# Performance work log

Measured on AMD Instinct MI355X. Metric: run time of the kernel, lower is better.

Reference implementation:

```python
import jax, jax.numpy as jnp
import numpy as np

B, N, P_FEATS = 8, 4096, 3
WIDTH, HEADS, LAYERS, N_LAT = 768, 12, 8, 256
NUM_FREQS = 8
D_HEAD = WIDTH // HEADS
SCALE = 1.0 / np.sqrt(np.sqrt(D_HEAD))  # applied to q and k separately
IN_DIM = 3 * (1 + 2 * NUM_FREQS) + P_FEATS  # 54
EPS = 1e-5


def fourier_embed(pc):
    # pc: [B,N,3] -> [B,N,51] (include_input + sin/cos at freqs 2^0..2^7)
    freqs = (2.0 ** jnp.arange(NUM_FREQS)).astype(pc.dtype)
    ang = pc[..., None] * freqs  # [B,N,3,F]
    ang = ang.reshape(*pc.shape[:-1], 3 * NUM_FREQS)
    return jnp.concatenate([pc, jnp.sin(ang), jnp.cos(ang)], axis=-1)


def layernorm(x, s, b):
    mu = jnp.mean(x, axis=-1, keepdims=True)
    var = jnp.mean(jnp.square(x - mu), axis=-1, keepdims=True)
    return (x - mu) * jax.lax.rsqrt(var + EPS) * s + b


def mh_attn(q, k, v):
    # q: [B,T,H,C], k/v: [B,S,H,C]
    w = jnp.einsum('bthc,bshc->bhts', q * SCALE, k * SCALE)
    w = jax.nn.softmax(w.astype(jnp.float32), axis=-1).astype(q.dtype)
    out = jnp.einsum('bhts,bshc->bthc', w, v)
    return out.reshape(*q.shape[:2], -1)


def setup_inputs() -> dict:
    key = jax.random.key(0)
    ks = iter(jax.random.split(key, 64))
    rn = lambda shape, std=0.02: jax.random.normal(next(ks), shape, jnp.float32) * std
    inp = {
        'pc': jax.random.normal(next(ks), (B, N, 3), jnp.float32),
        'feats': jax.random.uniform(next(ks), (B, N, P_FEATS), jnp.float32),
        'query': rn((N_LAT, WIDTH)),
        'in_W': rn((WIDTH, IN_DIM)), 'in_b': jnp.zeros((WIDTH,)),
        'ca_qkv_W': rn((3 * WIDTH, WIDTH)), 'ca_qkv_b': jnp.zeros((3 * WIDTH,)),
        'ca_proj_W': rn((WIDTH, WIDTH)), 'ca_proj_b': jnp.zeros((WIDTH,)),
        'ln1_s': jnp.ones((LAYERS, WIDTH)), 'ln1_b': jnp.zeros((LAYERS, WIDTH)),
        'qkv_W': rn((LAYERS, 3 * WIDTH, WIDTH)), 'qkv_b': jnp.zeros((LAYERS, 3 * WIDTH)),
        'proj_W': rn((LAYERS, WIDTH, WIDTH)), 'proj_b': jnp.zeros((LAYERS, WIDTH)),
        'ln2_s': jnp.ones((LAYERS, WIDTH)), 'ln2_b': jnp.zeros((LAYERS, WIDTH)),
        'fc_W': rn((LAYERS, 4 * WIDTH, WIDTH)), 'fc_b': jnp.zeros((LAYERS, 4 * WIDTH)),
        'fc2_W': rn((LAYERS, WIDTH, 4 * WIDTH)), 'fc2_b': jnp.zeros((LAYERS, WIDTH)),
    }
    return inp


def _forward(pc, feats, query, in_W, in_b, ca_qkv_W, ca_qkv_b, ca_proj_W, ca_proj_b,
             ln1_s, ln1_b, qkv_W, qkv_b, proj_W, proj_b, ln2_s, ln2_b,
             fc_W, fc_b, fc2_W, fc2_b):
    bs = pc.shape[0]
    data = jnp.concatenate([fourier_embed(pc), feats], axis=-1)  # [B,N,54]
    data = data @ in_W.T + in_b  # [B,N,W]
    q_lat = jnp.broadcast_to(query[None], (bs, N_LAT, WIDTH))

    # --- cross attention (no residual, matching source) ---
    q = (q_lat @ ca_qkv_W.T + ca_qkv_b)[..., :WIDTH]
    kv = data @ ca_qkv_W.T + ca_qkv_b
    k, v = kv[..., WIDTH:2 * WIDTH], kv[..., 2 * WIDTH:]
    q = q.reshape(bs, N_LAT, HEADS, D_HEAD)
    k = k.reshape(bs, N, HEADS, D_HEAD)
    v = v.reshape(bs, N, HEADS, D_HEAD)
    latents = mh_attn(q, k, v) @ ca_proj_W.T + ca_proj_b  # [B,L,W]

    # --- self-attention transformer stack via scan ---
    def block(x, p):
        (l1s, l1b, qW, qb, pW, pb, l2s, l2b, fW, fb, f2W, f2b) = p
        h = layernorm(x, l1s, l1b)
        qkv = (h @ qW.T + qb).reshape(bs, N_LAT, HEADS, 3 * D_HEAD)
        qh, kh, vh = jnp.split(qkv, 3, axis=-1)
        x = x + mh_attn(qh, kh, vh) @ pW.T + pb
        h = layernorm(x, l2s, l2b)
        h = jax.nn.gelu(h @ fW.T + fb, approximate=False) @ f2W.T + f2b
        return x + h, None

    params = (ln1_s, ln1_b, qkv_W, qkv_b, proj_W, proj_b, ln2_s, ln2_b, fc_W, fc_b, fc2_W, fc2_b)
    latents, _ = jax.lax.scan(block, latents, params)
    return latents, pc


def reference(pc, feats, query, in_W, in_b, ca_qkv_W, ca_qkv_b, ca_proj_W, ca_proj_b,
              ln1_s, ln1_b, qkv_W, qkv_b, proj_W, proj_b, ln2_s, ln2_b,
              fc_W, fc_b, fc2_W, fc2_b):
    return _forward(pc, feats, query, in_W, in_b, ca_qkv_W, ca_qkv_b, ca_proj_W, ca_proj_b,
                    ln1_s, ln1_b, qkv_W, qkv_b, proj_W, proj_b, ln2_s, ln2_b,
                    fc_W, fc_b, fc2_W, fc2_b)
```

## Files before the change

kernel.cpp:

```cpp
#include <hip/hip_runtime.h>
#include <stdint.h>

typedef unsigned short u16;
typedef __bf16 bf16x8 __attribute__((ext_vector_type(8)));
typedef float f32x4 __attribute__((ext_vector_type(4)));

#define DEVINL __device__ __forceinline__

DEVINL u16 f2bf(float f) {
  union { float f; unsigned u; } c; c.f = f;
  unsigned u = c.u + 0x7FFFu + ((c.u >> 16) & 1u);
  return (u16)(u >> 16);
}

DEVINL float bf2f(u16 v) {
  union { unsigned u; float f; } c; c.u = (unsigned)v << 16;
  return c.f;
}

DEVINL unsigned pk2bf(float a, float b) {
#if __has_builtin(__builtin_amdgcn_cvt_pk_bf16_f32)
  auto r = __builtin_amdgcn_cvt_pk_bf16_f32(a, b);
  unsigned u;
  __builtin_memcpy(&u, &r, 4);
  return u;
#else
  return (unsigned)f2bf(a) | ((unsigned)f2bf(b) << 16);
#endif
}

DEVINL void gl2lds16(const void* g, void* l) {
  __builtin_amdgcn_global_load_lds(
      (const __attribute__((address_space(1))) unsigned int*)g,
      (__attribute__((address_space(3))) unsigned int*)l, 16, 0, 0);
}

__global__ __launch_bounds__(256) void cvt4_kernel(
    const float* __restrict__ s0, u16* __restrict__ d0, int n0,
    const float* __restrict__ s1, u16* __restrict__ d1, int n1,
    const float* __restrict__ s2, u16* __restrict__ d2, int n2,
    const float* __restrict__ s3, u16* __restrict__ d3, int n3) {
  int i = blockIdx.x * 256 + threadIdx.x;
  const float* s; u16* d;
  if (i < n0) { s = s0; d = d0; }
  else {
    i -= n0;
    if (i < n1) { s = s1; d = d1; }
    else {
      i -= n1;
      if (i < n2) { s = s2; d = d2; }
      else {
        i -= n2;
        if (i >= n3) return;
        s = s3; d = d3;
      }
    }
  }
  float4 v = ((const float4*)s)[i];
  ((uint2*)d)[i] = make_uint2(pk2bf(v.x, v.y), pk2bf(v.z, v.w));
}

__global__ __launch_bounds__(256) void pad_inwT_kernel(const float* __restrict__ src,
                                                       u16* __restrict__ dst) {
  int t = blockIdx.x * 256 + threadIdx.x;
  if (t >= 64 * 768) return;
  int j = t / 768, o = t - j * 768;
  dst[t] = (j < 54) ? f2bf(src[o * 54 + j]) : (u16)0;
}

__global__ __launch_bounds__(256) void bprime_kernel(const float* __restrict__ caW,
                                                     const float* __restrict__ caB,
                                                     const float* __restrict__ inb,
                                                     float* __restrict__ bp) {
  int w = threadIdx.x >> 6, lane = threadIdx.x & 63;
  int m = blockIdx.x * 4 + w;
  const float* row = caW + (size_t)(768 + m) * 768;
  float s = 0.f;
#pragma unroll
  for (int k = 0; k < 12; k++) s += row[lane + k * 64] * inb[lane + k * 64];
#pragma unroll
  for (int msk = 32; msk >= 1; msk >>= 1) s += __shfl_xor(s, msk, 64);
  if (lane == 0) bp[m] = s + caB[768 + m];
}

__global__ __launch_bounds__(256) void embed_kernel(const float* __restrict__ pc,
                                                    const float* __restrict__ feats,
                                                    u16* __restrict__ emb) {
  int t = blockIdx.x * 256 + threadIdx.x;
  int p = t >> 6, c = t & 63;
  float v = 0.f;
  if (c < 3) {
    v = pc[p * 3 + c];
  } else if (c < 27) {
    int i = c - 3;
    float f = (float)(1 << (i & 7));
    v = sinf(pc[p * 3 + (i >> 3)] * f);
  } else if (c < 51) {
    int i = c - 27;
    float f = (float)(1 << (i & 7));
    v = cosf(pc[p * 3 + (i >> 3)] * f);
  } else if (c < 54) {
    v = feats[p * 3 + (c - 51)];
  }
  emb[t] = f2bf(v);
}

template <int TM, int TN, int WR, int WC, int MODE>
__global__ __launch_bounds__(256) void gemm_t(
    const u16* __restrict__ A, const u16* __restrict__ Bw,
    const float* __restrict__ bias, const float* __restrict__ resid,
    float* __restrict__ outF, u16* __restrict__ outB,
    int M, int N, int Nout, int K, int gelu,
    u16* __restrict__ vt, int vy, int skvt, int bsh) {
  constexpr int IM = TM / WR / 16;
  constexpr int IN = TN / WC / 16;
  __shared__ u16 As[TM * 32];
  __shared__ u16 Bs[TN * 32];
  const int tid = threadIdx.x;
  const int lane = tid & 63, w = tid >> 6;
  const int l15 = lane & 15, quad = lane >> 4;
  const int mblk = blockIdx.x * TM, nblk = blockIdx.y * TN;
  const int wm = (w % WR) * (TM / WR);
  const int wn = (w / WR) * (TN / WC);

  f32x4 acc[IM][IN];
#pragma unroll
  for (int i = 0; i < IM; i++)
#pragma unroll
    for (int j = 0; j < IN; j++) acc[i][j] = f32x4{0.f, 0.f, 0.f, 0.f};

  bool tv = false;
  if (MODE == 1) tv = ((int)blockIdx.y >= vy);
  if (MODE == 2) tv = ((int)(blockIdx.y % 3) == 2);

  if (!tv) {
    for (int k0 = 0; k0 < K; k0 += 32) {
#pragma unroll
      for (int s = tid; s < TM * 4; s += 256) {
        int row = s >> 2, c8 = (s & 3) << 3;
        gl2lds16(A + (size_t)(mblk + row) * K + (k0 + c8), &As[s * 8]);
      }
#pragma unroll
      for (int s = tid; s < TN * 4; s += 256) {
        int row = s >> 2, c8 = (s & 3) << 3;
        gl2lds16(Bw + (size_t)(nblk + row) * K + (k0 + c8), &Bs[s * 8]);
      }
      __syncthreads();
      bf16x8 af[IM], bfr[IN];
#pragma unroll
      for (int i = 0; i < IM; i++)
        af[i] = *(const bf16x8*)&As[(wm + i * 16 + l15) * 32 + quad * 8];
#pragma unroll
      for (int j = 0; j < IN; j++)
        bfr[j] = *(const bf16x8*)&Bs[(wn + j * 16 + l15) * 32 + quad * 8];
#pragma unroll
      for (int i = 0; i < IM; i++)
#pragma unroll
        for (int j = 0; j < IN; j++)
          acc[i][j] = __builtin_amdgcn_mfma_f32_16x16x32_bf16(bfr[j], af[i], acc[i][j], 0, 0, 0);
      __syncthreads();
    }
#pragma unroll
    for (int i = 0; i < IM; i++) {
      int m = mblk + wm + i * 16 + l15;
#pragma unroll
      for (int j = 0; j < IN; j++) {
        int n0 = nblk + wn + j * 16 + quad * 4;
        float4 bv = bias ? *(const float4*)&bias[n0] : make_float4(0.f, 0.f, 0.f, 0.f);
        float v0 = acc[i][j][0] + bv.x;
        float v1 = acc[i][j][1] + bv.y;
        float v2 = acc[i][j][2] + bv.z;
        float v3 = acc[i][j][3] + bv.w;
        if (gelu) {
          v0 = 0.5f * v0 * (1.0f + erff(v0 * 0.70710678118f));
          v1 = 0.5f * v1 * (1.0f + erff(v1 * 0.70710678118f));
          v2 = 0.5f * v2 * (1.0f + erff(v2 * 0.70710678118f));
          v3 = 0.5f * v3 * (1.0f + erff(v3 * 0.70710678118f));
        }
        size_t idx = (size_t)m * Nout + n0;
        if (resid) {
          float4 rv = *(const float4*)&resid[idx];
          v0 += rv.x; v1 += rv.y; v2 += rv.z; v3 += rv.w;
        }
        if (outF) {
          float4 ov = {v0, v1, v2, v3};
          *(float4*)&outF[idx] = ov;
        }
        if (outB) {
          *(uint2*)&outB[idx] = make_uint2(pk2bf(v0, v1), pk2bf(v2, v3));
        }
      }
    }
  } else {
    for (int k0 = 0; k0 < K; k0 += 32) {
#pragma unroll
      for (int s = tid; s < TM * 4; s += 256) {
        int row = s >> 2, c8 = (s & 3) << 3;
        gl2lds16(A + (size_t)(mblk + row) * K + (k0 + c8), &As[s * 8]);
      }
#pragma unroll
      for (int s = tid; s < TN * 4; s += 256) {
        int row = s >> 2, c8 = (s & 3) << 3;
        gl2lds16(Bw + (size_t)(nblk + row) * K + (k0 + c8), &Bs[s * 8]);
      }
      __syncthreads();
      bf16x8 af[IM], bfr[IN];
#pragma unroll
      for (int i = 0; i < IM; i++)
        af[i] = *(const bf16x8*)&As[(wm + i * 16 + l15) * 32 + quad * 8];
#pragma unroll
      for (int j = 0; j < IN; j++)
        bfr[j] = *(const bf16x8*)&Bs[(wn + j * 16 + l15) * 32 + quad * 8];
#pragma unroll
      for (int i = 0; i < IM; i++)
#pragma unroll
        for (int j = 0; j < IN; j++)
          acc[i][j] = __builtin_amdgcn_mfma_f32_16x16x32_bf16(af[i], bfr[j], acc[i][j], 0, 0, 0);
      __syncthreads();
    }
    int msk = (1 << bsh) - 1;
#pragma unroll
    for (int j = 0; j < IN; j++) {
      int n = nblk + wn + j * 16 + l15;
      float bv = bias ? bias[n] : 0.f;
#pragma unroll
      for (int i = 0; i < IM; i++) {
        int m0 = mblk + wm + i * 16 + quad * 4;
        int b = m0 >> bsh;
        int s0 = m0 & msk;
        float v0 = acc[i][j][0] + bv;
        float v1 = acc[i][j][1] + bv;
        float v2 = acc[i][j][2] + bv;
        float v3 = acc[i][j][3] + bv;
        size_t vrow;
        if (MODE == 2) {
          int h = blockIdx.y / 3;
          vrow = (size_t)(b * 12 + h) * 64 + (wn + j * 16 + l15);
        } else {
          vrow = (size_t)b * 768 + (n - vy * TN);
        }
        size_t addr = vrow * skvt + s0;
        *(uint2*)&vt[addr] = make_uint2(pk2bf(v0, v1), pk2bf(v2, v3));
      }
    }
  }
}

__global__ __launch_bounds__(256) void flash_kernel(
    const u16* __restrict__ Q, long qb, int qrs, int qhs,
    const u16* __restrict__ Kp, long kb, int krs, int khs,
    const u16* __restrict__ Vt, u16* __restrict__ Out,
    u16* __restrict__ Part, float* __restrict__ Ml,
    int Skv, int nsplit, int kvlen, int nbh, float scale2) {
  __shared__ u16 Qs[64 * 64];
  __shared__ u16 Ks[64 * 64];
  __shared__ u16 Vs[64 * 64];
  __shared__ u16 Ps[64 * 72];

  const int tid = threadIdx.x;
  const int lane = tid & 63, w = tid >> 6;
  const int l15 = lane & 15, quad = lane >> 4;

  int bid = blockIdx.x;
  int grp = nbh * nsplit;
  int qt = bid / grp;
  int rem = bid - qt * grp;
  int bh = rem / nsplit;
  int split = rem - bh * nsplit;
  int h = bh % 12, b = bh / 12;

  const u16* Qbase = Q + (size_t)b * qb + (size_t)(qt * 64) * qrs + h * qhs;
  const u16* Kbase = Kp + (size_t)b * kb + (size_t)h * khs;
  const u16* Vbase = Vt + ((size_t)(b * 12 + h) * 64) * Skv;

#pragma unroll
  for (int p = 0; p < 2; ++p) {
    int slot = tid + p * 256;
    int row = slot >> 3, c = slot & 7;
    int cg = (c - row) & 7;
    gl2lds16(Qbase + (size_t)row * qrs + cg * 8, &Qs[slot * 8]);
  }
  __syncthreads();

  bf16x8 qa[2];
#pragma unroll
  for (int kk = 0; kk < 2; kk++)
    qa[kk] = *(const bf16x8*)&Qs[(w * 16 + l15) * 64 + ((kk * 4 + quad + l15) & 7) * 8];

  f32x4 zero = {0.f, 0.f, 0.f, 0.f};
  f32x4 O[4];
#pragma unroll
  for (int d = 0; d < 4; d++) O[d] = zero;
  float m_i = -1e30f, l_i = 0.f;

  int kt0 = split * kvlen;
  for (int kt = kt0; kt < kt0 + kvlen; kt += 64) {
#pragma unroll
    for (int p = 0; p < 2; ++p) {
      int slot = tid + p * 256;
      int row = slot >> 3, c = slot & 7;
      int cg = (c - row) & 7;
      gl2lds16(Kbase + (size_t)(kt + row) * krs + cg * 8, &Ks[slot * 8]);
      gl2lds16(Vbase + (size_t)row * Skv + kt + cg * 8, &Vs[slot * 8]);
    }
    __syncthreads();

    f32x4 St[4];
#pragma unroll
    for (int j = 0; j < 4; j++) St[j] = zero;
#pragma unroll
    for (int kk = 0; kk < 2; kk++) {
#pragma unroll
      for (int j = 0; j < 4; j++) {
        bf16x8 kf = *(const bf16x8*)&Ks[(j * 16 + l15) * 64 + ((kk * 4 + quad + l15) & 7) * 8];
        St[j] = __builtin_amdgcn_mfma_f32_16x16x32_bf16(kf, qa[kk], St[j], 0, 0, 0);
      }
    }

    float mx = St[0][0];
#pragma unroll
    for (int j = 0; j < 4; j++)
#pragma unroll
      for (int r = 0; r < 4; r++) mx = fmaxf(mx, St[j][r]);
    mx = fmaxf(mx, __shfl_xor(mx, 16, 64));
    mx = fmaxf(mx, __shfl_xor(mx, 32, 64));
    mx *= scale2;
    float mnew = fmaxf(m_i, mx);
    float al = __expf(m_i - mnew);
    m_i = mnew;
    float sum = 0.f;
#pragma unroll
    for (int j = 0; j < 4; j++) {
      float p0 = __expf(fmaf(St[j][0], scale2, -mnew));
      float p1 = __expf(fmaf(St[j][1], scale2, -mnew));
      float p2 = __expf(fmaf(St[j][2], scale2, -mnew));
      float p3 = __expf(fmaf(St[j][3], scale2, -mnew));
      sum += (p0 + p1) + (p2 + p3);
      *(uint2*)&Ps[(w * 16 + l15) * 72 + j * 16 + quad * 4] =
          make_uint2(pk2bf(p0, p1), pk2bf(p2, p3));
    }
    sum += __shfl_xor(sum, 16, 64);
    sum += __shfl_xor(sum, 32, 64);
    l_i = l_i * al + sum;

    float a0 = __shfl(al, quad * 20 + 0, 64);
    float a1 = __shfl(al, quad * 20 + 1, 64);
    float a2 = __shfl(al, quad * 20 + 2, 64);
    float a3 = __shfl(al, quad * 20 + 3, 64);
#pragma unroll
    for (int d = 0; d < 4; d++) {
      O[d][0] *= a0; O[d][1] *= a1; O[d][2] *= a2; O[d][3] *= a3;
    }
    __asm__ __volatile__("s_waitcnt lgkmcnt(0)" ::: "memory");
#pragma unroll
    for (int kk = 0; kk < 2; kk++) {
      bf16x8 pa = *(const bf16x8*)&Ps[(w * 16 + l15) * 72 + kk * 32 + quad * 8];
#pragma unroll
      for (int d = 0; d < 4; d++) {
        bf16x8 vf = *(const bf16x8*)&Vs[(d * 16 + l15) * 64 + ((kk * 4 + quad + l15) & 7) * 8];
        O[d] = __builtin_amdgcn_mfma_f32_16x16x32_bf16(pa, vf, O[d], 0, 0, 0);
      }
    }
    __syncthreads();
  }

  float l0 = __shfl(l_i, quad * 20 + 0, 64);
  float l1 = __shfl(l_i, quad * 20 + 1, 64);
  float l2 = __shfl(l_i, quad * 20 + 2, 64);
  float l3 = __shfl(l_i, quad * 20 + 3, 64);

  if (nsplit == 1) {
    float inv0 = 1.f / l0, inv1 = 1.f / l1, inv2 = 1.f / l2, inv3 = 1.f / l3;
    u16* Ob = Out + ((size_t)(b * 256 + qt * 64 + w * 16 + quad * 4)) * 768 + h * 64 + l15;
#pragma unroll
    for (int d = 0; d < 4; d++) {
      Ob[(size_t)0 * 768 + d * 16] = f2bf(O[d][0] * inv0);
      Ob[(size_t)1 * 768 + d * 16] = f2bf(O[d][1] * inv1);
      Ob[(size_t)2 * 768 + d * 16] = f2bf(O[d][2] * inv2);
      Ob[(size_t)3 * 768 + d * 16] = f2bf(O[d][3] * inv3);
    }
  } else {
    float m0 = __shfl(m_i, quad * 20 + 0, 64);
    float m1 = __shfl(m_i, quad * 20 + 1, 64);
    float m2 = __shfl(m_i, quad * 20 + 2, 64);
    float m3 = __shfl(m_i, quad * 20 + 3, 64);
    u16* Pb = Part + ((size_t)(bh * 4 + qt) * nsplit + split) * 4096;
    int rowb = w * 16 + quad * 4;
#pragma unroll
    for (int d = 0; d < 4; d++) {
      Pb[(rowb + 0) * 64 + d * 16 + l15] = f2bf(O[d][0]);
      Pb[(rowb + 1) * 64 + d * 16 + l15] = f2bf(O[d][1]);
      Pb[(rowb + 2) * 64 + d * 16 + l15] = f2bf(O[d][2]);
      Pb[(rowb + 3) * 64 + d * 16 + l15] = f2bf(O[d][3]);
    }
    if (l15 == 0) {
      float* MlB = Ml + ((size_t)(bh * 4 + qt) * nsplit + split) * 128;
      MlB[rowb + 0] = m0; MlB[rowb + 1] = m1; MlB[rowb + 2] = m2; MlB[rowb + 3] = m3;
      MlB[64 + rowb + 0] = l0; MlB[64 + rowb + 1] = l1;
      MlB[64 + rowb + 2] = l2; MlB[64 + rowb + 3] = l3;
    }
  }
}

__global__ __launch_bounds__(256) void freduce_kernel(
    const u16* __restrict__ Part, const float* __restrict__ Ml,
    u16* __restrict__ Out, int nsplit) {
  int bid = blockIdx.x;
  int qt = bid & 3, bh = bid >> 2;
  int h = bh % 12, b = bh / 12;
  int tid = threadIdx.x;
  int r = tid >> 2, dc = tid & 3;
  const float* mlb = Ml + (size_t)(bh * 4 + qt) * nsplit * 128;
  float M = -1e30f;
  for (int s = 0; s < nsplit; s++) M = fmaxf(M, mlb[s * 128 + r]);
  float L = 0.f;
  float accv[16];
#pragma unroll
  for (int i = 0; i < 16; i++) accv[i] = 0.f;
  const u16* pb = Part + (size_t)(bh * 4 + qt) * nsplit * 4096 + r * 64 + dc * 16;
  for (int s = 0; s < nsplit; s++) {
    float wgt = __expf(mlb[s * 128 + r] - M);
    L += wgt * mlb[s * 128 + 64 + r];
    u16 tmp[16];
    *(uint4*)tmp = *(const uint4*)(pb + s * 4096);
    *(uint4*)(tmp + 8) = *(const uint4*)(pb + s * 4096 + 8);
#pragma unroll
    for (int i = 0; i < 16; i++) accv[i] += wgt * bf2f(tmp[i]);
  }
  float inv = 1.f / L;
  unsigned ot[8];
#pragma unroll
  for (int i = 0; i < 8; i++)
    ot[i] = pk2bf(accv[2 * i] * inv, accv[2 * i + 1] * inv);
  u16* ob = Out + ((size_t)(b * 256 + qt * 64 + r)) * 768 + h * 64 + dc * 16;
  *(uint4*)ob = *(uint4*)ot;
  *(uint4*)(ob + 8) = *(uint4*)(ot + 4);
}

__global__ __launch_bounds__(256) void ln_kernel(const float* __restrict__ X,
                                                 const float* __restrict__ sc,
                                                 const float* __restrict__ bi,
                                                 u16* __restrict__ Hout) {
  int row = blockIdx.x;
  int tid = threadIdx.x;
  const float* x = X + (size_t)row * 768;
  float v0 = x[tid], v1 = x[tid + 256], v2 = x[tid + 512];
  float s = v0 + v1 + v2;
  float q = v0 * v0 + v1 * v1 + v2 * v2;
#pragma unroll
  for (int m = 1; m < 64; m <<= 1) {
    s += __shfl_xor(s, m, 64);
    q += __shfl_xor(q, m, 64);
  }
  __shared__ float rs[4], rq[4];
  if ((tid & 63) == 0) { rs[tid >> 6] = s; rq[tid >> 6] = q; }
  __syncthreads();
  s = rs[0] + rs[1] + rs[2] + rs[3];
  q = rq[0] + rq[1] + rq[2] + rq[3];
  float mu = s * (1.f / 768.f);
  float var = q * (1.f / 768.f) - mu * mu;
  float rstd = rsqrtf(var + 1e-5f);
  u16* ho = Hout + (size_t)row * 768;
  ho[tid]       = f2bf((v0 - mu) * rstd * sc[tid]       + bi[tid]);
  ho[tid + 256] = f2bf((v1 - mu) * rstd * sc[tid + 256] + bi[tid + 256]);
  ho[tid + 512] = f2bf((v2 - mu) * rstd * sc[tid + 512] + bi[tid + 512]);
}

__global__ __launch_bounds__(256) void copy4_kernel(const float* __restrict__ src,
                                                    float* __restrict__ dst, int n4) {
  int i = blockIdx.x * 256 + threadIdx.x;
  if (i < n4) ((float4*)dst)[i] = ((const float4*)src)[i];
}

extern "C" void kernel_launch(void* const* d_in, const int* in_sizes, int n_in,
                              void* d_out, int out_size, void* d_ws, size_t ws_size,
                              hipStream_t stream) {
  const float* pc        = (const float*)d_in[0];
  const float* feats     = (const float*)d_in[1];
  const float* query     = (const float*)d_in[2];
  const float* in_W      = (const float*)d_in[3];
  const float* in_b      = (const float*)d_in[4];
  const float* ca_qkv_W  = (const float*)d_in[5];
  const float* ca_qkv_b  = (const float*)d_in[6];
  const float* ca_proj_W = (const float*)d_in[7];
  const float* ca_proj_b = (const float*)d_in[8];
  const float* ln1_s     = (const float*)d_in[9];
  const float* ln1_b     = (const float*)d_in[10];
  const float* qkv_W     = (const float*)d_in[11];
  const float* qkv_b     = (const float*)d_in[12];
  const float* proj_W    = (const float*)d_in[13];
  const float* proj_b    = (const float*)d_in[14];
  const float* ln2_s     = (const float*)d_in[15];
  const float* ln2_b     = (const float*)d_in[16];
  const float* fc_W      = (const float*)d_in[17];
  const float* fc_b      = (const float*)d_in[18];
  const float* fc2_W     = (const float*)d_in[19];
  const float* fc2_b     = (const float*)d_in[20];

  char* base = (char*)d_ws;
  size_t off = 0;
  auto alloc = [&](size_t bytes) -> char* {
    char* p = base + off;
    off += (bytes + 255) & ~(size_t)255;
    return p;
  };

  u16* WqT     = (u16*)alloc(64 * 768 * 2);
  u16* Wquery  = (u16*)alloc(256 * 768 * 2);
  u16* Wcaqkv  = (u16*)alloc(2304 * 768 * 2);
  u16* Wcaproj = (u16*)alloc(768 * 768 * 2);
  u16* Wkp     = (u16*)alloc(1536 * 64 * 2);
  float* bprime = (float*)alloc(1536 * 4);
  u16* qc      = (u16*)alloc(256 * 768 * 2);
  u16* attn    = (u16*)alloc((size_t)2048 * 768 * 2);
  u16* hbuf    = (u16*)alloc((size_t)2048 * 768 * 2);
  char* uni    = alloc(13369344);
  u16* qkvb    = (u16*)uni;
  u16* VtS     = (u16*)(uni + 9437184);
  u16* fc1     = (u16*)uni;
  u16* Part    = (u16*)uni;
  float* Ml    = (float*)(uni + 12582912);

  size_t fixed_end = off;
  const size_t wAllSz = (size_t)8 * (2304 * 768 + 768 * 768 + 2 * 3072 * 768) * 2;
  auto crossSz = [](int cb) {
    return (size_t)cb * 4096 * 64 * 2 + 2 * ((size_t)cb * 4096 * 768 * 2);
  };

  bool allw; int CB;
  if (fixed_end + (wAllSz > crossSz(8) ? wAllSz : crossSz(8)) + 65536 <= ws_size) {
    allw = true;  CB = 8;
  } else if (fixed_end + 14155776 + crossSz(2) + 65536 <= ws_size) {
    allw = false; CB = 2;
  } else {
    allw = false; CB = 1;
  }

  u16 *WqkvB, *WprojB, *WfcB, *Wfc2B, *emb, *kvbK, *VtC;
  if (allw) {
    char* X = base + off;
    WqkvB  = (u16*)X;
    WprojB = WqkvB + (size_t)8 * 2304 * 768;
    WfcB   = WprojB + (size_t)8 * 768 * 768;
    Wfc2B  = WfcB + (size_t)8 * 3072 * 768;
    emb  = (u16*)X;
    kvbK = (u16*)(X + (size_t)CB * 4096 * 64 * 2);
    VtC  = (u16*)(X + (size_t)CB * 4096 * 64 * 2 + (size_t)CB * 4096 * 768 * 2);
  } else {
    WqkvB  = (u16*)alloc(2304 * 768 * 2);
    WprojB = (u16*)alloc(768 * 768 * 2);
    WfcB   = (u16*)alloc(3072 * 768 * 2);
    Wfc2B  = (u16*)alloc((size_t)768 * 3072 * 2);
    emb  = (u16*)alloc((size_t)CB * 4096 * 64 * 2);
    kvbK = (u16*)alloc((size_t)CB * 4096 * 768 * 2);
    VtC  = (u16*)alloc((size_t)CB * 4096 * 768 * 2);
  }

  float* latents = (float*)d_out;
  const float scale2 = 0.125f;

  {
    int n0 = 256 * 768 / 4, n1 = 2304 * 768 / 4, n2 = 768 * 768 / 4;
    cvt4_kernel<<<(n0 + n1 + n2 + 255) / 256, 256, 0, stream>>>(
        query, Wquery, n0, ca_qkv_W, Wcaqkv, n1, ca_proj_W, Wcaproj, n2,
        nullptr, nullptr, 0);
  }
  pad_inwT_kernel<<<192, 256, 0, stream>>>(in_W, WqT);
  gemm_t<64, 64, 2, 2, 0><<<dim3(24, 1), 256, 0, stream>>>(
      Wcaqkv + (size_t)768 * 768, WqT, nullptr, nullptr, nullptr, Wkp,
      1536, 64, 64, 768, 0, nullptr, 0, 0, 0);
  bprime_kernel<<<384, 256, 0, stream>>>(ca_qkv_W, ca_qkv_b, in_b, bprime);

  gemm_t<64, 64, 2, 2, 0><<<dim3(4, 12), 256, 0, stream>>>(
      Wquery, Wcaqkv, ca_qkv_b, nullptr, nullptr, qc,
      256, 768, 768, 768, 0, nullptr, 0, 0, 0);

  int nchunk = 8 / CB;
  for (int c = 0; c < nchunk; ++c) {
    int Mc = CB * 4096;
    const float* pc_c = pc + (size_t)c * Mc * 3;
    const float* ft_c = feats + (size_t)c * Mc * 3;
    embed_kernel<<<Mc / 4, 256, 0, stream>>>(pc_c, ft_c, emb);
    gemm_t<128, 128, 2, 2, 1><<<dim3(Mc / 128, 12), 256, 0, stream>>>(
        emb, Wkp, bprime, nullptr, nullptr, kvbK,
        Mc, 1536, 768, 64, 0, VtC, 6, 4096, 12);
    flash_kernel<<<CB * 12 * 16, 256, 0, stream>>>(
        qc, 0L, 768, 64, kvbK, (long)4096 * 768, 768, 64, VtC,
        nullptr, Part, Ml, 4096, 4, 1024, CB * 12, scale2);
    freduce_kernel<<<CB * 48, 256, 0, stream>>>(
        Part, Ml, attn + (size_t)c * CB * 256 * 768, 4);
  }
  gemm_t<64, 64, 2, 2, 0><<<dim3(32, 12), 256, 0, stream>>>(
      attn, Wcaproj, ca_proj_b, nullptr, latents, nullptr,
      2048, 768, 768, 768, 0, nullptr, 0, 0, 0);

  if (allw) {
    int n0 = 8 * 2304 * 768 / 4, n1 = 8 * 768 * 768 / 4, n2 = 8 * 3072 * 768 / 4;
    cvt4_kernel<<<(n0 + n1 + 2 * n2 + 255) / 256, 256, 0, stream>>>(
        qkv_W, WqkvB, n0, proj_W, WprojB, n1, fc_W, WfcB, n2, fc2_W, Wfc2B, n2);
  }

  for (int l = 0; l < 8; ++l) {
    u16* Wlq  = allw ? WqkvB  + (size_t)l * 2304 * 768 : WqkvB;
    u16* Wlp  = allw ? WprojB + (size_t)l * 768 * 768  : WprojB;
    u16* Wlf  = allw ? WfcB   + (size_t)l * 3072 * 768 : WfcB;
    u16* Wlf2 = allw ? Wfc2B  + (size_t)l * 3072 * 768 : Wfc2B;
    if (!allw) {
      int n0 = 2304 * 768 / 4, n1 = 768 * 768 / 4, n2 = 3072 * 768 / 4;
      cvt4_kernel<<<(n0 + n1 + 2 * n2 + 255) / 256, 256, 0, stream>>>(
          qkv_W + (size_t)l * 2304 * 768, Wlq, n0,
          proj_W + (size_t)l * 768 * 768, Wlp, n1,
          fc_W + (size_t)l * 3072 * 768, Wlf, n2,
          fc2_W + (size_t)l * 768 * 3072, Wlf2, n2);
    }
    ln_kernel<<<2048, 256, 0, stream>>>(latents, ln1_s + l * 768, ln1_b + l * 768, hbuf);
    gemm_t<64, 64, 2, 2, 2><<<dim3(32, 36), 256, 0, stream>>>(
        hbuf, Wlq, qkv_b + l * 2304, nullptr, nullptr, qkvb,
        2048, 2304, 2304, 768, 0, VtS, 0, 256, 8);
    flash_kernel<<<384, 256, 0, stream>>>(
        qkvb, (long)256 * 2304, 2304, 192, qkvb + 64, (long)256 * 2304, 2304, 192,
        VtS, attn, nullptr, nullptr, 256, 1, 256, 96, scale2);
    gemm_t<64, 64, 2, 2, 0><<<dim3(32, 12), 256, 0, stream>>>(
        attn, Wlp, proj_b + l * 768, latents, latents, nullptr,
        2048, 768, 768, 768, 0, nullptr, 0, 0, 0);
    ln_kernel<<<2048, 256, 0, stream>>>(latents, ln2_s + l * 768, ln2_b + l * 768, hbuf);
    gemm_t<64, 128, 1, 4, 0><<<dim3(32, 24), 256, 0, stream>>>(
        hbuf, Wlf, fc_b + l * 3072, nullptr, nullptr, fc1,
        2048, 3072, 3072, 768, 1, nullptr, 0, 0, 0);
    gemm_t<64, 64, 2, 2, 0><<<dim3(32, 12), 256, 0, stream>>>(
        fc1, Wlf2, fc2_b + l * 768, latents, latents, nullptr,
        2048, 768, 768, 3072, 0, nullptr, 0, 0, 0);
  }

  copy4_kernel<<<96, 256, 0, stream>>>(pc, (float*)d_out + (size_t)2048 * 768, 98304 / 4);
}
```

Before: 1.333 ms.

## Add split-K GEMMs for narrow projections and double-buffer flash attention K/V

```diff
diff --git a/kernel.cpp b/kernel.cpp
--- a/kernel.cpp
+++ b/kernel.cpp
@@ -33,6 +33,15 @@
   __builtin_amdgcn_global_load_lds(
       (const __attribute__((address_space(1))) unsigned int*)g,
       (__attribute__((address_space(3))) unsigned int*)l, 16, 0, 0);
+}
+
+template <int N> DEVINL void waitvm() {
+  asm volatile("s_waitcnt vmcnt(%0)" ::"n"(N) : "memory");
+}
+DEVINL void bar() {
+  asm volatile("" ::: "memory");
+  __builtin_amdgcn_s_barrier();
+  asm volatile("" ::: "memory");
 }
 
 __global__ __launch_bounds__(256) void cvt4_kernel(
@@ -246,6 +255,93 @@
   }
 }
 
+template <int TM, int TN, int WR, int WC>
+__global__ __launch_bounds__(256) void gemmsk_t(
+    const u16* __restrict__ A, const u16* __restrict__ Bw,
+    float* __restrict__ P, int M, int N, int K, int kchunk) {
+  constexpr int IM = TM / WR / 16;
+  constexpr int IN = TN / WC / 16;
+  __shared__ u16 As[TM * 32];
+  __shared__ u16 Bs[TN * 32];
+  const int tid = threadIdx.x;
+  const int lane = tid & 63, w = tid >> 6;
+  const int l15 = lane & 15, quad = lane >> 4;
+  const int mblk = blockIdx.x * TM, nblk = blockIdx.y * TN;
+  const int wm = (w % WR) * (TM / WR);
+  const int wn = (w / WR) * (TN / WC);
+  const int kbeg = blockIdx.z * kchunk;
+  const int kend = kbeg + kchunk;
+
+  f32x4 acc[IM][IN];
+#pragma unroll
+  for (int i = 0; i < IM; i++)
+#pragma unroll
+    for (int j = 0; j < IN; j++) acc[i][j] = f32x4{0.f, 0.f, 0.f, 0.f};
+
+  for (int k0 = kbeg; k0 < kend; k0 += 32) {
+#pragma unroll
+    for (int s = tid; s < TM * 4; s += 256) {
+      int row = s >> 2, c8 = (s & 3) << 3;
+      gl2lds16(A + (size_t)(mblk + row) * K + (k0 + c8), &As[s * 8]);
+    }
+#pragma unroll
+    for (int s = tid; s < TN * 4; s += 256) {
+      int row = s >> 2, c8 = (s & 3) << 3;
+      gl2lds16(Bw + (size_t)(nblk + row) * K + (k0 + c8), &Bs[s * 8]);
+    }
+    __syncthreads();
+    bf16x8 af[IM], bfr[IN];
+#pragma unroll
+    for (int i = 0; i < IM; i++)
+      af[i] = *(const bf16x8*)&As[(wm + i * 16 + l15) * 32 + quad * 8];
+#pragma unroll
+    for (int j = 0; j < IN; j++)
+      bfr[j] = *(const bf16x8*)&Bs[(wn + j * 16 + l15) * 32 + quad * 8];
+#pragma unroll
+    for (int i = 0; i < IM; i++)
+#pragma unroll
+      for (int j = 0; j < IN; j++)
+        acc[i][j] = __builtin_amdgcn_mfma_f32_16x16x32_bf16(bfr[j], af[i], acc[i][j], 0, 0, 0);
+    __syncthreads();
+  }
+
+  float* Pz = P + (size_t)blockIdx.z * M * N;
+#pragma unroll
+  for (int i = 0; i < IM; i++) {
+    int m = mblk + wm + i * 16 + l15;
+#pragma unroll
+    for (int j = 0; j < IN; j++) {
+      int n0 = nblk + wn + j * 16 + quad * 4;
+      float4 ov = {acc[i][j][0], acc[i][j][1], acc[i][j][2], acc[i][j][3]};
+      *(float4*)&Pz[(size_t)m * N + n0] = ov;
+    }
+  }
+}
+
+__global__ __launch_bounds__(256) void skred_kernel(
+    const float* __restrict__ P, int nsk, int MN4, int N,
+    const float* __restrict__ bias, const float* __restrict__ resid,
+    float* __restrict__ outF, u16* __restrict__ outB) {
+  int i = blockIdx.x * 256 + threadIdx.x;
+  if (i >= MN4) return;
+  float4 s = ((const float4*)P)[i];
+  for (int z = 1; z < nsk; z++) {
+    float4 t = ((const float4*)P)[(size_t)z * MN4 + i];
+    s.x += t.x; s.y += t.y; s.z += t.z; s.w += t.w;
+  }
+  if (bias) {
+    int n0 = (i * 4) % N;
+    float4 b = *(const float4*)&bias[n0];
+    s.x += b.x; s.y += b.y; s.z += b.z; s.w += b.w;
+  }
+  if (resid) {
+    float4 r = ((const float4*)resid)[i];
+    s.x += r.x; s.y += r.y; s.z += r.z; s.w += r.w;
+  }
+  if (outF) ((float4*)outF)[i] = s;
+  if (outB) ((uint2*)outB)[i] = make_uint2(pk2bf(s.x, s.y), pk2bf(s.z, s.w));
+}
+
 __global__ __launch_bounds__(256) void flash_kernel(
     const u16* __restrict__ Q, long qb, int qrs, int qhs,
     const u16* __restrict__ Kp, long kb, int krs, int khs,
@@ -253,8 +349,8 @@
     u16* __restrict__ Part, float* __restrict__ Ml,
     int Skv, int nsplit, int kvlen, int nbh, float scale2) {
   __shared__ u16 Qs[64 * 64];
-  __shared__ u16 Ks[64 * 64];
-  __shared__ u16 Vs[64 * 64];
+  __shared__ u16 Ks[2][64 * 64];
+  __shared__ u16 Vs[2][64 * 64];
   __shared__ u16 Ps[64 * 72];
 
   const int tid = threadIdx.x;
@@ -273,12 +369,16 @@
   const u16* Kbase = Kp + (size_t)b * kb + (size_t)h * khs;
   const u16* Vbase = Vt + ((size_t)(b * 12 + h) * 64) * Skv;
 
+  int kt0 = split * kvlen;
+
 #pragma unroll
   for (int p = 0; p < 2; ++p) {
     int slot = tid + p * 256;
     int row = slot >> 3, c = slot & 7;
     int cg = (c - row) & 7;
     gl2lds16(Qbase + (size_t)row * qrs + cg * 8, &Qs[slot * 8]);
+    gl2lds16(Kbase + (size_t)(kt0 + row) * krs + cg * 8, &Ks[0][slot * 8]);
+    gl2lds16(Vbase + (size_t)row * Skv + kt0 + cg * 8, &Vs[0][slot * 8]);
   }
   __syncthreads();
 
@@ -293,17 +393,23 @@
   for (int d = 0; d < 4; d++) O[d] = zero;
   float m_i = -1e30f, l_i = 0.f;
 
-  int kt0 = split * kvlen;
+  int cur = 0;
   for (int kt = kt0; kt < kt0 + kvlen; kt += 64) {
-#pragma unroll
-    for (int p = 0; p < 2; ++p) {
-      int slot = tid + p * 256;
-      int row = slot >> 3, c = slot & 7;
-      int cg = (c - row) & 7;
-      gl2lds16(Kbase + (size_t)(kt + row) * krs + cg * 8, &Ks[slot * 8]);
-      gl2lds16(Vbase + (size_t)row * Skv + kt + cg * 8, &Vs[slot * 8]);
-    }
-    __syncthreads();
+    bool hasnext = (kt + 64 < kt0 + kvlen);
+    if (hasnext) {
+#pragma unroll
+      for (int p = 0; p < 2; ++p) {
+        int slot = tid + p * 256;
+        int row = slot >> 3, c = slot & 7;
+        int cg = (c - row) & 7;
+        gl2lds16(Kbase + (size_t)(kt + 64 + row) * krs + cg * 8, &Ks[cur ^ 1][slot * 8]);
+        gl2lds16(Vbase + (size_t)row * Skv + (kt + 64) + cg * 8, &Vs[cur ^ 1][slot * 8]);
+      }
+      waitvm<4>();
+    } else {
+      waitvm<0>();
+    }
+    bar();
 
     f32x4 St[4];
 #pragma unroll
@@ -312,7 +418,7 @@
     for (int kk = 0; kk < 2; kk++) {
 #pragma unroll
       for (int j = 0; j < 4; j++) {
-        bf16x8 kf = *(const bf16x8*)&Ks[(j * 16 + l15) * 64 + ((kk * 4 + quad + l15) & 7) * 8];
+        bf16x8 kf = *(const bf16x8*)&Ks[cur][(j * 16 + l15) * 64 + ((kk * 4 + quad + l15) & 7) * 8];
         St[j] = __builtin_amdgcn_mfma_f32_16x16x32_bf16(kf, qa[kk], St[j], 0, 0, 0);
       }
     }
@@ -325,31 +431,41 @@
     mx = fmaxf(mx, __shfl_xor(mx, 16, 64));
     mx = fmaxf(mx, __shfl_xor(mx, 32, 64));
     mx *= scale2;
-    float mnew = fmaxf(m_i, mx);
-    float al = __expf(m_i - mnew);
-    m_i = mnew;
+
+    bool skip = __all(mx <= m_i + 8.f);
+    float al = 1.f;
+    if (!skip) {
+      float mnew = fmaxf(m_i, mx);
+      al = __expf(m_i - mnew);
+      m_i = mnew;
+    }
+    float mref = m_i;
     float sum = 0.f;
 #pragma unroll
     for (int j = 0; j < 4; j++) {
-      float p0 = __expf(fmaf(St[j][0], scale2, -mnew));
-      float p1 = __expf(fmaf(St[j][1], scale2, -mnew));
-      float p2 = __expf(fmaf(St[j][2], scale2, -mnew));
-      float p3 = __expf(fmaf(St[j][3], scale2, -mnew));
+      float p0 = __expf(fmaf(St[j][0], scale2, -mref));
+      float p1 = __expf(fmaf(St[j][1], scale2, -mref));
+      float p2 = __expf(fmaf(St[j][2], scale2, -mref));
+      float p3 = __expf(fmaf(St[j][3], scale2, -mref));
       sum += (p0 + p1) + (p2 + p3);
       *(uint2*)&Ps[(w * 16 + l15) * 72 + j * 16 + quad * 4] =
           make_uint2(pk2bf(p0, p1), pk2bf(p2, p3));
     }
     sum += __shfl_xor(sum, 16, 64);
     sum += __shfl_xor(sum, 32, 64);
-    l_i = l_i * al + sum;
-
-    float a0 = __shfl(al, quad * 20 + 0, 64);
-    float a1 = __shfl(al, quad * 20 + 1, 64);
-    float a2 = __shfl(al, quad * 20 + 2, 64);
-    float a3 = __shfl(al, quad * 20 + 3, 64);
-#pragma unroll
-    for (int d = 0; d < 4; d++) {
-      O[d][0] *= a0; O[d][1] *= a1; O[d][2] *= a2; O[d][3] *= a3;
+
+    if (skip) {
+      l_i += sum;
+    } else {
+      l_i = l_i * al + sum;
+      float a0 = __shfl(al, quad * 20 + 0, 64);
+      float a1 = __shfl(al, quad * 20 + 1, 64);
+      float a2 = __shfl(al, quad * 20 + 2, 64);
+      float a3 = __shfl(al, quad * 20 + 3, 64);
+#pragma unroll
+      for (int d = 0; d < 4; d++) {
+        O[d][0] *= a0; O[d][1] *= a1; O[d][2] *= a2; O[d][3] *= a3;
+      }
     }
     __asm__ __volatile__("s_waitcnt lgkmcnt(0)" ::: "memory");
 #pragma unroll
@@ -357,11 +473,12 @@
       bf16x8 pa = *(const bf16x8*)&Ps[(w * 16 + l15) * 72 + kk * 32 + quad * 8];
 #pragma unroll
       for (int d = 0; d < 4; d++) {
-        bf16x8 vf = *(const bf16x8*)&Vs[(d * 16 + l15) * 64 + ((kk * 4 + quad + l15) & 7) * 8];
+        bf16x8 vf = *(const bf16x8*)&Vs[cur][(d * 16 + l15) * 64 + ((kk * 4 + quad + l15) & 7) * 8];
         O[d] = __builtin_amdgcn_mfma_f32_16x16x32_bf16(pa, vf, O[d], 0, 0, 0);
       }
     }
-    __syncthreads();
+    bar();
+    cur ^= 1;
   }
 
   float l0 = __shfl(l_i, quad * 20 + 0, 64);
@@ -546,6 +663,7 @@
     emb  = (u16*)X;
     kvbK = (u16*)(X + (size_t)CB * 4096 * 64 * 2);
     VtC  = (u16*)(X + (size_t)CB * 4096 * 64 * 2 + (size_t)CB * 4096 * 768 * 2);
+    off = fixed_end + (wAllSz > crossSz(8) ? wAllSz : crossSz(8));
   } else {
     WqkvB  = (u16*)alloc(2304 * 768 * 2);
     WprojB = (u16*)alloc(768 * 768 * 2);
@@ -556,6 +674,13 @@
     VtC  = (u16*)alloc((size_t)CB * 4096 * 768 * 2);
   }
 
+  const size_t pb2048 = (size_t)2048 * 768 * 4;
+  auto fits = [&](size_t bytes) { return off + bytes + 4096 <= ws_size; };
+  int nsk_fc2 = fits(4 * pb2048) ? 4 : (fits(2 * pb2048) ? 2 : 1);
+  int nsk_pr  = fits(2 * pb2048) ? 2 : 1;
+  int nsk_qc  = fits((size_t)256 * 768 * 4 * 8) ? 8 : 1;
+  float* skP  = (float*)(base + off);
+
   float* latents = (float*)d_out;
   const float scale2 = 0.125f;
 
@@ -571,9 +696,16 @@
       1536, 64, 64, 768, 0, nullptr, 0, 0, 0);
   bprime_kernel<<<384, 256, 0, stream>>>(ca_qkv_W, ca_qkv_b, in_b, bprime);
 
-  gemm_t<64, 64, 2, 2, 0><<<dim3(4, 12), 256, 0, stream>>>(
-      Wquery, Wcaqkv, ca_qkv_b, nullptr, nullptr, qc,
-      256, 768, 768, 768, 0, nullptr, 0, 0, 0);
+  if (nsk_qc > 1) {
+    gemmsk_t<64, 64, 2, 2><<<dim3(4, 12, nsk_qc), 256, 0, stream>>>(
+        Wquery, Wcaqkv, skP, 256, 768, 768, 768 / nsk_qc);
+    skred_kernel<<<192, 256, 0, stream>>>(
+        skP, nsk_qc, 256 * 768 / 4, 768, ca_qkv_b, nullptr, nullptr, qc);
+  } else {
+    gemm_t<64, 64, 2, 2, 0><<<dim3(4, 12), 256, 0, stream>>>(
+        Wquery, Wcaqkv, ca_qkv_b, nullptr, nullptr, qc,
+        256, 768, 768, 768, 0, nullptr, 0, 0, 0);
+  }
 
   int nchunk = 8 / CB;
   for (int c = 0; c < nchunk; ++c) {
@@ -590,9 +722,16 @@
     freduce_kernel<<<CB * 48, 256, 0, stream>>>(
         Part, Ml, attn + (size_t)c * CB * 256 * 768, 4);
   }
-  gemm_t<64, 64, 2, 2, 0><<<dim3(32, 12), 256, 0, stream>>>(
-      attn, Wcaproj, ca_proj_b, nullptr, latents, nullptr,
-      2048, 768, 768, 768, 0, nullptr, 0, 0, 0);
+  if (nsk_pr > 1) {
+    gemmsk_t<64, 64, 2, 2><<<dim3(32, 12, nsk_pr), 256, 0, stream>>>(
+        attn, Wcaproj, skP, 2048, 768, 768, 768 / nsk_pr);
+    skred_kernel<<<1536, 256, 0, stream>>>(
+        skP, nsk_pr, 2048 * 768 / 4, 768, ca_proj_b, nullptr, latents, nullptr);
+  } else {
+    gemm_t<64, 64, 2, 2, 0><<<dim3(32, 12), 256, 0, stream>>>(
+        attn, Wcaproj, ca_proj_b, nullptr, latents, nullptr,
+        2048, 768, 768, 768, 0, nullptr, 0, 0, 0);
+  }
 
   if (allw) {
     int n0 = 8 * 2304 * 768 / 4, n1 = 8 * 768 * 768 / 4, n2 = 8 * 3072 * 768 / 4;
@@ -620,16 +759,30 @@
     flash_kernel<<<384, 256, 0, stream>>>(
         qkvb, (long)256 * 2304, 2304, 192, qkvb + 64, (long)256 * 2304, 2304, 192,
         VtS, attn, nullptr, nullptr, 256, 1, 256, 96, scale2);
-    gemm_t<64, 64, 2, 2, 0><<<dim3(32, 12), 256, 0, stream>>>(
-        attn, Wlp, proj_b + l * 768, latents, latents, nullptr,
-        2048, 768, 768, 768, 0, nullptr, 0, 0, 0);
+    if (nsk_pr > 1) {
+      gemmsk_t<64, 64, 2, 2><<<dim3(32, 12, nsk_pr), 256, 0, stream>>>(
+          attn, Wlp, skP, 2048, 768, 768, 768 / nsk_pr);
+      skred_kernel<<<1536, 256, 0, stream>>>(
+          skP, nsk_pr, 2048 * 768 / 4, 768, proj_b + l * 768, latents, latents, nullptr);
+    } else {
+      gemm_t<64, 64, 2, 2, 0><<<dim3(32, 12), 256, 0, stream>>>(
+          attn, Wlp, proj_b + l * 768, latents, latents, nullptr,
+          2048, 768, 768, 768, 0, nullptr, 0, 0, 0);
+    }
     ln_kernel<<<2048, 256, 0, stream>>>(latents, ln2_s + l * 768, ln2_b + l * 768, hbuf);
     gemm_t<64, 128, 1, 4, 0><<<dim3(32, 24), 256, 0, stream>>>(
         hbuf, Wlf, fc_b + l * 3072, nullptr, nullptr, fc1,
         2048, 3072, 3072, 768, 1, nullptr, 0, 0, 0);
-    gemm_t<64, 64, 2, 2, 0><<<dim3(32, 12), 256, 0, stream>>>(
-        fc1, Wlf2, fc2_b + l * 768, latents, latents, nullptr,
-        2048, 768, 768, 3072, 0, nullptr, 0, 0, 0);
+    if (nsk_fc2 > 1) {
+      gemmsk_t<64, 64, 2, 2><<<dim3(32, 12, nsk_fc2), 256, 0, stream>>>(
+          fc1, Wlf2, skP, 2048, 768, 3072, 3072 / nsk_fc2);
+      skred_kernel<<<1536, 256, 0, stream>>>(
+          skP, nsk_fc2, 2048 * 768 / 4, 768, fc2_b + l * 768, latents, latents, nullptr);
+    } else {
+      gemm_t<64, 64, 2, 2, 0><<<dim3(32, 12), 256, 0, stream>>>(
+          fc1, Wlf2, fc2_b + l * 768, latents, latents, nullptr,
+          2048, 768, 768, 3072, 0, nullptr, 0, 0, 0);
+    }
   }
 
   copy4_kernel<<<96, 256, 0, stream>>>(pc, (float*)d_out + (size_t)2048 * 768, 98304 / 4);
```

Result: faster. 1.293 ms (-3.0%).
